# Kernel optimization log

Hardware: AMD Instinct MI355X
Metric: run time of the kernel (lower is better)

The kernel has to match this reference:

```python
import jax, jax.numpy as jnp
import numpy as np

# Static problem sizes (must match input construction)
B, G, EPG, K, C = 64, 24, 512, 20, 1
NS = B * G            # total number of subgraphs
E = NS * EPG          # total number of edges
M, H = 4096, 256      # node_state shape


def setup_inputs() -> dict:
    key = jax.random.key(0)
    ks = jax.random.split(key, 8)
    label = (jax.random.uniform(ks[0], (E,)) < 0.5).astype(jnp.float32)
    label0 = (jax.random.uniform(ks[1], (E,)) < 0.5).astype(jnp.float32)
    log_theta = jax.random.normal(ks[2], (E, K), dtype=jnp.float32)
    log_theta0 = jax.random.normal(ks[3], (E, K), dtype=jnp.float32)
    log_alpha = jax.random.normal(ks[4], (E, K), dtype=jnp.float32)
    log_alpha0 = jax.random.normal(ks[5], (E, K), dtype=jnp.float32)
    subgraph_idx = (jnp.arange(E, dtype=jnp.int32) // EPG).astype(jnp.int32)
    subgraph_idx0 = subgraph_idx
    subgraph_idx_base = (jnp.arange(B + 1, dtype=jnp.int32) * (G * C)).astype(jnp.int32)
    subgraph_idx_base0 = subgraph_idx_base
    node_state = jax.random.normal(ks[6], (M, H), dtype=jnp.float32)
    node_state0 = jax.random.normal(ks[7], (M, H), dtype=jnp.float32)
    return {
        "label": label, "label0": label0,
        "log_theta": log_theta, "log_theta0": log_theta0,
        "log_alpha": log_alpha, "log_alpha0": log_alpha0,
        "subgraph_idx": subgraph_idx, "subgraph_idx0": subgraph_idx0,
        "subgraph_idx_base": subgraph_idx_base, "subgraph_idx_base0": subgraph_idx_base0,
        "node_state": node_state, "node_state0": node_state0,
    }


def _bce_with_logits(logits, y):
    # BCEWithLogitsLoss(reduction='none'), broadcast label over K mixture components
    return -(y[:, None] * jax.nn.log_sigmoid(logits)
             + (1.0 - y)[:, None] * jax.nn.log_sigmoid(-logits))


def _stream_loss(label, log_theta, log_alpha, subgraph_idx, subgraph_idx_base):
    adj_loss = _bce_with_logits(log_theta, label)                     # E x K
    const = jax.ops.segment_sum(jnp.ones((E,), jnp.float32), subgraph_idx, NS)  # edges per subgraph
    reduce_adj_loss = jax.ops.segment_sum(adj_loss, subgraph_idx, NS)  # NS x K
    reduce_log_alpha = jax.ops.segment_sum(log_alpha, subgraph_idx, NS) / const[:, None]
    reduce_log_alpha = jax.nn.log_softmax(reduce_log_alpha, axis=-1)
    log_prob = jax.nn.logsumexp(-reduce_adj_loss + reduce_log_alpha, axis=1)  # NS
    # bc_idx: map each subgraph to its (batch, canonical-order) slot; C == 1 here,
    # equivalent to repeat_interleave(arange(B*C), bc_size) in the original.
    bc_idx = jnp.searchsorted(subgraph_idx_base, jnp.arange(NS, dtype=jnp.int32), side='right') - 1
    bc_log_prob = jax.ops.segment_sum(log_prob, bc_idx, B * C).reshape(B, C)
    bc_const = jax.ops.segment_sum(const, bc_idx, B * C).reshape(B, C)
    bc_loss = bc_log_prob / bc_const
    b_loss = jax.nn.logsumexp(bc_loss, axis=1)   # sum_order_log_prob=False
    return jnp.mean(-b_loss)                      # reduction='mean'


def _trace_cdist(ns, ns0):
    # Fused replacement for the naive O(m^2) host-side pairwise-distance loop:
    # D[i,j] = ||ns[i] - ns0[j]||, then trace(D).
    x2 = jnp.sum(ns * ns, axis=1)
    y2 = jnp.sum(ns0 * ns0, axis=1)
    d2 = x2[:, None] + y2[None, :] - 2.0 * (ns @ ns0.T)   # M x M
    D = jnp.sqrt(jnp.maximum(d2, 0.0))
    return jnp.trace(D)


def reference(label, label0, log_theta, log_theta0, log_alpha, log_alpha0,
              subgraph_idx, subgraph_idx0, subgraph_idx_base, subgraph_idx_base0,
              node_state, node_state0):
    loss = _stream_loss(label, log_theta, log_alpha, subgraph_idx, subgraph_idx_base)
    loss0 = _stream_loss(label0, log_theta0, log_alpha0, subgraph_idx0, subgraph_idx_base0)
    trD = _trace_cdist(node_state, node_state0)
    # return_neg_log_prob=False branch of the original
    return 10.0 * (loss + loss0) + trD
```

## Files before the change

### kernel.cpp

```cpp
#include <hip/hip_runtime.h>
#include <math.h>

#define B_   64
#define G_   24
#define EPG_ 512
#define K_   20
#define NS_  (B_ * G_)
#define E_   (NS_ * EPG_)
#define M_   4096
#define H_   256

#define NT_  320
#define F4_  (EPG_ * K_ / 4)
#define IT_  (F4_ / NT_)

__global__ __launch_bounds__(NT_)
void stream_loss_kernel(const float* __restrict__ label,
                        const float* __restrict__ label0,
                        const float* __restrict__ log_theta,
                        const float* __restrict__ log_theta0,
                        const float* __restrict__ log_alpha,
                        const float* __restrict__ log_alpha0,
                        float* __restrict__ out)
{
    const int s   = blockIdx.x;
    const int tid = threadIdx.x;

    const float* lab = (blockIdx.y == 0) ? label     : label0;
    const float4* lt4 = (const float4*)((blockIdx.y == 0) ? log_theta : log_theta0);
    const float4* la4 = (const float4*)((blockIdx.y == 0) ? log_alpha : log_alpha0);

    __shared__ float  s_label[EPG_];
    __shared__ float4 red_adj[NT_];
    __shared__ float4 red_alpha[NT_];
    __shared__ float  S_adj[K_];
    __shared__ float  S_alpha[K_];

    {
        const float4* labp4 = (const float4*)(lab + (size_t)s * EPG_);
        if (tid < EPG_ / 4) ((float4*)s_label)[tid] = labp4[tid];
    }
    __syncthreads();

    const int e_div = tid / 5;

    float4 acc_adj   = make_float4(0.f, 0.f, 0.f, 0.f);
    float4 acc_alpha = make_float4(0.f, 0.f, 0.f, 0.f);

    const size_t base4 = (size_t)s * F4_;
    #pragma unroll
    for (int i = 0; i < IT_; ++i) {
        const float y = s_label[i * 64 + e_div];
        const size_t f = base4 + (size_t)i * NT_ + tid;
        const float4 x = lt4[f];
        const float4 a = la4[f];
        acc_adj.x += fmaxf(x.x, 0.f) - x.x * y + __logf(1.f + __expf(-fabsf(x.x)));
        acc_adj.y += fmaxf(x.y, 0.f) - x.y * y + __logf(1.f + __expf(-fabsf(x.y)));
        acc_adj.z += fmaxf(x.z, 0.f) - x.z * y + __logf(1.f + __expf(-fabsf(x.z)));
        acc_adj.w += fmaxf(x.w, 0.f) - x.w * y + __logf(1.f + __expf(-fabsf(x.w)));
        acc_alpha.x += a.x;
        acc_alpha.y += a.y;
        acc_alpha.z += a.z;
        acc_alpha.w += a.w;
    }
    red_adj[tid]   = acc_adj;
    red_alpha[tid] = acc_alpha;
    __syncthreads();

    if (tid < K_) {
        const int q = tid >> 2;
        const int j = tid & 3;
        float sa = 0.0f, sl = 0.0f;
        #pragma unroll
        for (int m = 0; m < 64; ++m) {
            const int t = m * 5 + q;
            sa += ((const float*)&red_adj[t])[j];
            sl += ((const float*)&red_alpha[t])[j];
        }
        S_adj[tid]   = sa;
        S_alpha[tid] = sl;
    }
    __syncthreads();

    if (tid == 0) {
        const float inv_const = 1.0f / (float)EPG_;
        float m1 = -INFINITY;
        #pragma unroll
        for (int i = 0; i < K_; ++i) m1 = fmaxf(m1, S_alpha[i] * inv_const);
        float sum1 = 0.0f;
        #pragma unroll
        for (int i = 0; i < K_; ++i) sum1 += __expf(S_alpha[i] * inv_const - m1);
        const float lse = m1 + __logf(sum1);

        float m2 = -INFINITY;
        #pragma unroll
        for (int i = 0; i < K_; ++i) {
            const float v = -S_adj[i] + S_alpha[i] * inv_const - lse;
            m2 = fmaxf(m2, v);
        }
        float sum2 = 0.0f;
        #pragma unroll
        for (int i = 0; i < K_; ++i) {
            const float v = -S_adj[i] + S_alpha[i] * inv_const - lse;
            sum2 += __expf(v - m2);
        }
        const float lp = m2 + __logf(sum2);

        atomicAdd(out, lp * (-10.0f / (float)E_));
    }
}

__global__ __launch_bounds__(256)
void trace_cdist_kernel(const float* __restrict__ ns,
                        const float* __restrict__ ns0,
                        float* __restrict__ out)
{
    const int wave = threadIdx.x >> 6;
    const int lane = threadIdx.x & 63;
    __shared__ float s_d[16];

    #pragma unroll
    for (int i = 0; i < 4; ++i) {
        const int row = blockIdx.x * 16 + wave * 4 + i;
        const float4* a = (const float4*)(ns  + (size_t)row * H_);
        const float4* b = (const float4*)(ns0 + (size_t)row * H_);
        const float4 av = a[lane];
        const float4 bv = b[lane];
        const float dx = av.x - bv.x;
        const float dy = av.y - bv.y;
        const float dz = av.z - bv.z;
        const float dw = av.w - bv.w;
        float sv = dx * dx + dy * dy + dz * dz + dw * dw;
        #pragma unroll
        for (int off = 32; off > 0; off >>= 1) sv += __shfl_down(sv, off);
        if (lane == 0) s_d[wave * 4 + i] = sqrtf(sv);
    }
    __syncthreads();
    if (threadIdx.x == 0) {
        float t = 0.0f;
        #pragma unroll
        for (int i = 0; i < 16; ++i) t += s_d[i];
        atomicAdd(out, t);
    }
}

extern "C" void kernel_launch(void* const* d_in, const int* in_sizes, int n_in,
                              void* d_out, int out_size, void* d_ws, size_t ws_size,
                              hipStream_t stream) {
    const float* label       = (const float*)d_in[0];
    const float* label0      = (const float*)d_in[1];
    const float* log_theta   = (const float*)d_in[2];
    const float* log_theta0  = (const float*)d_in[3];
    const float* log_alpha   = (const float*)d_in[4];
    const float* log_alpha0  = (const float*)d_in[5];
    const float* node_state  = (const float*)d_in[10];
    const float* node_state0 = (const float*)d_in[11];
    float* out = (float*)d_out;

    hipMemsetAsync(out, 0, sizeof(float), stream);

    dim3 grid(NS_, 2);
    stream_loss_kernel<<<grid, NT_, 0, stream>>>(label, label0,
                                                 log_theta, log_theta0,
                                                 log_alpha, log_alpha0, out);
    trace_cdist_kernel<<<M_ / 16, 256, 0, stream>>>(node_state, node_state0, out);
}
```

Before: 268.0 us.

## Prefetch stream-loss inputs into registers and tree-reduce partial sums

All log_theta and log_alpha float4 loads for a block are issued up front into register arrays, so they overlap with the label staging and the first barrier instead of being interleaved with the math. The serial 64-step per-component reduction over shared memory is replaced by a halving tree (160→20) followed by a 4-way final sum. A min-blocks hint of 5 is added to launch bounds. This raises register pressure from holding IT_ float4 pairs per thread and adds several barriers in the reduction.

```diff
diff --git a/kernel.cpp b/kernel.cpp
--- a/kernel.cpp
+++ b/kernel.cpp
@@ -14,7 +14,7 @@
 #define F4_  (EPG_ * K_ / 4)
 #define IT_  (F4_ / NT_)
 
-__global__ __launch_bounds__(NT_)
+__global__ __launch_bounds__(NT_, 5)
 void stream_loss_kernel(const float* __restrict__ label,
                         const float* __restrict__ label0,
                         const float* __restrict__ log_theta,
@@ -26,7 +26,7 @@
     const int s   = blockIdx.x;
     const int tid = threadIdx.x;
 
-    const float* lab = (blockIdx.y == 0) ? label     : label0;
+    const float*  lab = (blockIdx.y == 0) ? label     : label0;
     const float4* lt4 = (const float4*)((blockIdx.y == 0) ? log_theta : log_theta0);
     const float4* la4 = (const float4*)((blockIdx.y == 0) ? log_alpha : log_alpha0);
 
@@ -36,24 +36,29 @@
     __shared__ float  S_adj[K_];
     __shared__ float  S_alpha[K_];
 
-    {
-        const float4* labp4 = (const float4*)(lab + (size_t)s * EPG_);
-        if (tid < EPG_ / 4) ((float4*)s_label)[tid] = labp4[tid];
-    }
+    float4 labv;
+    if (tid < EPG_ / 4)
+        labv = ((const float4*)(lab + (size_t)s * EPG_))[tid];
+
+    const size_t base4 = (size_t)s * F4_ + tid;
+    float4 xv[IT_], av[IT_];
+    #pragma unroll
+    for (int i = 0; i < IT_; ++i) xv[i] = lt4[base4 + (size_t)i * NT_];
+    #pragma unroll
+    for (int i = 0; i < IT_; ++i) av[i] = la4[base4 + (size_t)i * NT_];
+
+    if (tid < EPG_ / 4)
+        ((float4*)s_label)[tid] = labv;
     __syncthreads();
 
     const int e_div = tid / 5;
-
     float4 acc_adj   = make_float4(0.f, 0.f, 0.f, 0.f);
     float4 acc_alpha = make_float4(0.f, 0.f, 0.f, 0.f);
-
-    const size_t base4 = (size_t)s * F4_;
     #pragma unroll
     for (int i = 0; i < IT_; ++i) {
         const float y = s_label[i * 64 + e_div];
-        const size_t f = base4 + (size_t)i * NT_ + tid;
-        const float4 x = lt4[f];
-        const float4 a = la4[f];
+        const float4 x = xv[i];
+        const float4 a = av[i];
         acc_adj.x += fmaxf(x.x, 0.f) - x.x * y + __logf(1.f + __expf(-fabsf(x.x)));
         acc_adj.y += fmaxf(x.y, 0.f) - x.y * y + __logf(1.f + __expf(-fabsf(x.y)));
         acc_adj.z += fmaxf(x.z, 0.f) - x.z * y + __logf(1.f + __expf(-fabsf(x.z)));
@@ -67,18 +72,30 @@
     red_alpha[tid] = acc_alpha;
     __syncthreads();
 
+    #pragma unroll
+    for (int half = 160; half >= 20; half >>= 1) {
+        if (tid < half) {
+            float4 a = red_adj[tid],   b = red_adj[tid + half];
+            a.x += b.x; a.y += b.y; a.z += b.z; a.w += b.w;
+            red_adj[tid] = a;
+            float4 c = red_alpha[tid], d = red_alpha[tid + half];
+            c.x += d.x; c.y += d.y; c.z += d.z; c.w += d.w;
+            red_alpha[tid] = c;
+        }
+        __syncthreads();
+    }
+
     if (tid < K_) {
         const int q = tid >> 2;
         const int j = tid & 3;
-        float sa = 0.0f, sl = 0.0f;
-        #pragma unroll
-        for (int m = 0; m < 64; ++m) {
-            const int t = m * 5 + q;
-            sa += ((const float*)&red_adj[t])[j];
-            sl += ((const float*)&red_alpha[t])[j];
-        }
-        S_adj[tid]   = sa;
-        S_alpha[tid] = sl;
+        S_adj[tid]   = ((const float*)&red_adj[q])[j]
+                     + ((const float*)&red_adj[q + 5])[j]
+                     + ((const float*)&red_adj[q + 10])[j]
+                     + ((const float*)&red_adj[q + 15])[j];
+        S_alpha[tid] = ((const float*)&red_alpha[q])[j]
+                     + ((const float*)&red_alpha[q + 5])[j]
+                     + ((const float*)&red_alpha[q + 10])[j]
+                     + ((const float*)&red_alpha[q + 15])[j];
     }
     __syncthreads();
 
```

After: 272.5 us. Within noise of the previous version (+1.7%).
